# Kernel optimization log

Measured on AMD Instinct MI355X. Metric: run time of the kernel, lower is better.

The kernel has to match this reference:

```python
import jax, jax.numpy as jnp
import numpy as np

B, T, E, NH, VOCAB, MULT = 1, 1024, 768, 12, 32000, 32
N = E * MULT // NH  # 2048
LN_EPS = 1e-5


def setup_inputs() -> dict:
    key = jax.random.key(0)
    ks = jax.random.split(key, 6)
    return {
        "idx": jax.random.randint(ks[0], (B, T), 0, VOCAB),
        "embed": jax.random.normal(ks[1], (VOCAB, E), jnp.float32) * 0.02,
        "encoder": jax.random.normal(ks[2], (NH, E, N), jnp.float32) * 0.02,
        "encoder_v": jax.random.normal(ks[3], (NH, E, N), jnp.float32) * 0.02,
        "decoder": jax.random.normal(ks[4], (NH * N, E), jnp.float32) * 0.02,
        "lm_head": jax.random.normal(ks[5], (VOCAB, E), jnp.float32) * 0.02,
        "ln_w": jnp.ones((E,), jnp.float32),
        "ln_b": jnp.zeros((E,), jnp.float32),
        "n_layer": 6,
    }


def reference(idx, embed, encoder, encoder_v, decoder, lm_head, ln_w, ln_b, n_layer):
    nh, e, n = encoder.shape
    t = idx.shape[1]
    dec = decoder.reshape(nh, n, e)  # flatten order (h, n) -> h*N + n

    def ln(x):
        m = jnp.mean(x, axis=-1, keepdims=True)
        v = jnp.mean(jnp.square(x - m), axis=-1, keepdims=True)
        return (x - m) * jax.lax.rsqrt(v + LN_EPS) * ln_w + ln_b

    causal = jnp.tril(jnp.ones((t, t), bool))  # [T, T]
    scale = 1.0 / np.sqrt(n).astype(np.float32)

    x = ln(embed[idx])  # [B, T, E]  (the unsqueezed head dim broadcasts; keep it squeezed)
    for _ in range(n_layer):
        # encoder projection + ReLU: [B,T,E] x [H,E,N] -> [B,H,T,N]
        x_sparse = jax.nn.relu(jnp.einsum("bte,hen->bhtn", x, encoder))
        # hand-rolled causal attention, Q=K=x_sparse, V=x (broadcast over heads)
        scores = jnp.einsum("bhqn,bhkn->bhqk", x_sparse, x_sparse) * scale
        scores = jnp.where(causal, scores, -jnp.inf)
        attn = jax.nn.softmax(scores, axis=-1)
        y = jnp.einsum("bhqk,bke->bhqe", attn, x)  # [B,H,T,E]
        y = ln(y)
        y_sparse = jax.nn.relu(jnp.einsum("bhte,hen->bhtn", y, encoder_v))
        xy = x_sparse * y_sparse  # [B,H,T,N]; dropout p=0 -> identity
        y_mlp = jnp.einsum("bhtn,hne->bte", xy, dec)  # decoder matmul
        x = ln(x + ln(y_mlp))
    logits = jnp.einsum("bte,ve->btv", x, lm_head)
    return logits
```

## Files before the change

kernel.cpp:

```cpp
#include <hip/hip_runtime.h>

typedef unsigned short u16;
typedef short bf16x8 __attribute__((ext_vector_type(8)));
typedef float f32x4 __attribute__((ext_vector_type(4)));
typedef u16 u16x4 __attribute__((ext_vector_type(4)));

#define TT     1024
#define EE     768
#define NHH    12
#define ND     2048
#define VOC    32000
#define HNN    24576
#define NLAYER 6
#define LN_EPS 1e-5f
#define SPLITK 16

__device__ __forceinline__ float b2f(u16 u){
  unsigned int x = ((unsigned int)u) << 16; float f; __builtin_memcpy(&f, &x, 4); return f;
}
__device__ __forceinline__ u16 f2b(float f){
  unsigned int x; __builtin_memcpy(&x, &f, 4);
  x = x + 0x7fffu + ((x >> 16) & 1u);
  return (u16)(x >> 16);
}

__device__ __forceinline__ void gload16(const void* g, void* lds){
  __builtin_amdgcn_global_load_lds(
      (const __attribute__((address_space(1))) unsigned int*)g,
      (__attribute__((address_space(3))) unsigned int*)(unsigned int)(unsigned long long)lds,
      16, 0, 0);
}

__device__ __forceinline__ bf16x8 ldsr(unsigned addr){
  bf16x8 r;
  asm volatile("ds_read_b128 %0, %1" : "=v"(r) : "v"(addr));
  return r;
}

__device__ __forceinline__ void blk_sum2(float& a, float& b){
  #pragma unroll
  for (int o = 32; o > 0; o >>= 1){ a += __shfl_down(a, o); b += __shfl_down(b, o); }
  __shared__ float sa[4], sb[4];
  int lane = threadIdx.x & 63, wid = threadIdx.x >> 6;
  __syncthreads();
  if (lane == 0){ sa[wid] = a; sb[wid] = b; }
  __syncthreads();
  a = (sa[0] + sa[1]) + (sa[2] + sa[3]);
  b = (sb[0] + sb[1]) + (sb[2] + sb[3]);
}
__device__ __forceinline__ float blk_max(float v){
  #pragma unroll
  for (int o = 32; o > 0; o >>= 1) v = fmaxf(v, __shfl_down(v, o));
  __shared__ float sm[4];
  int lane = threadIdx.x & 63, wid = threadIdx.x >> 6;
  __syncthreads();
  if (lane == 0) sm[wid] = v;
  __syncthreads();
  return fmaxf(fmaxf(sm[0], sm[1]), fmaxf(sm[2], sm[3]));
}
__device__ __forceinline__ float blk_sum(float v){
  #pragma unroll
  for (int o = 32; o > 0; o >>= 1) v += __shfl_down(v, o);
  __shared__ float ss[4];
  int lane = threadIdx.x & 63, wid = threadIdx.x >> 6;
  __syncthreads();
  if (lane == 0) ss[wid] = v;
  __syncthreads();
  return (ss[0] + ss[1]) + (ss[2] + ss[3]);
}

__global__ void transpose_f2b(const float* __restrict__ in, long sIn,
                              u16* __restrict__ out, long sOut, int R, int Cc){
  __shared__ float tile[32][33];
  int z = blockIdx.z;
  in  += (long)z * sIn;
  out += (long)z * sOut;
  int c0 = blockIdx.x * 32, r0 = blockIdx.y * 32;
  int lx = threadIdx.x & 31, ly = threadIdx.x >> 5;
  #pragma unroll
  for (int i = 0; i < 32; i += 8)
    tile[ly + i][lx] = in[(long)(r0 + ly + i) * Cc + (c0 + lx)];
  __syncthreads();
  #pragma unroll
  for (int i = 0; i < 32; i += 8)
    out[(long)(c0 + ly + i) * R + (r0 + lx)] = f2b(tile[lx][ly + i]);
}

__global__ void conv_f2b(const float* __restrict__ in, u16* __restrict__ out){
  long i = ((long)blockIdx.x * 256 + threadIdx.x) * 4;
  float4 v = *(const float4*)(in + i);
  u16x4 o; o.x = f2b(v.x); o.y = f2b(v.y); o.z = f2b(v.z); o.w = f2b(v.w);
  *(u16x4*)(out + i) = o;
}

__global__ void embed_ln(const int* __restrict__ idx, const float* __restrict__ emb,
                         const float* __restrict__ w, const float* __restrict__ b,
                         float* __restrict__ xf, u16* __restrict__ xb, u16* __restrict__ xT){
  int t = blockIdx.x, tid = threadIdx.x;
  const float* src = emb + (long)idx[t] * EE;
  float v[3];
  #pragma unroll
  for (int j = 0; j < 3; j++) v[j] = src[tid + j * 256];
  float s = v[0] + v[1] + v[2];
  float s2 = v[0]*v[0] + v[1]*v[1] + v[2]*v[2];
  blk_sum2(s, s2);
  float m  = s * (1.0f / EE);
  float var = s2 * (1.0f / EE) - m * m;
  float rs = rsqrtf(var + LN_EPS);
  #pragma unroll
  for (int j = 0; j < 3; j++){
    int e = tid + j * 256;
    float o = (v[j] - m) * rs * w[e] + b[e];
    xf[(long)t * EE + e] = o;
    u16 ob = f2b(o);
    xb[(long)t * EE + e] = ob;
    xT[(long)e * TT + t] = ob;
  }
}

__global__ void ln_rows(const float* __restrict__ in, u16* __restrict__ out,
                        const float* __restrict__ w, const float* __restrict__ b){
  long row = blockIdx.x; int tid = threadIdx.x;
  const float* src = in + row * EE;
  float v[3];
  #pragma unroll
  for (int j = 0; j < 3; j++) v[j] = src[tid + j * 256];
  float s = v[0] + v[1] + v[2];
  float s2 = v[0]*v[0] + v[1]*v[1] + v[2]*v[2];
  blk_sum2(s, s2);
  float m = s * (1.0f / EE);
  float var = s2 * (1.0f / EE) - m * m;
  float rs = rsqrtf(var + LN_EPS);
  #pragma unroll
  for (int j = 0; j < 3; j++){
    int e = tid + j * 256;
    out[row * EE + e] = f2b((v[j] - m) * rs * w[e] + b[e]);
  }
}

__global__ void softmax_rows(const float* __restrict__ scores, u16* __restrict__ attn){
  int q = blockIdx.x, h = blockIdx.y, tid = threadIdx.x;
  const float* srow = scores + ((long)h * TT + q) * TT;
  u16* arow = attn + ((long)h * TT + q) * TT;
  float4 v = *(const float4*)(srow + tid * 4);
  float mx = blk_max(fmaxf(fmaxf(v.x, v.y), fmaxf(v.z, v.w)));
  float e0 = __expf(v.x - mx), e1 = __expf(v.y - mx);
  float e2 = __expf(v.z - mx), e3 = __expf(v.w - mx);
  float inv = 1.0f / blk_sum(e0 + e1 + e2 + e3);
  u16x4 o; o.x = f2b(e0 * inv); o.y = f2b(e1 * inv); o.z = f2b(e2 * inv); o.w = f2b(e3 * inv);
  *(u16x4*)(arow + tid * 4) = o;
}

template<int P>
__global__ void residual_ln(const float* __restrict__ part, const float* __restrict__ xin,
                            float* __restrict__ xf, u16* __restrict__ xb, u16* __restrict__ xT,
                            const float* __restrict__ w, const float* __restrict__ b){
  int t = blockIdx.x, tid = threadIdx.x;
  float g[3];
  #pragma unroll
  for (int j = 0; j < 3; j++){
    int e = tid + j * 256;
    float s = 0.f;
    #pragma unroll
    for (int pp = 0; pp < P; pp++) s += part[((long)pp * TT + t) * EE + e];
    g[j] = s;
  }
  float s = g[0] + g[1] + g[2], s2 = g[0]*g[0] + g[1]*g[1] + g[2]*g[2];
  blk_sum2(s, s2);
  float m = s * (1.0f / EE), var = s2 * (1.0f / EE) - m * m;
  float rs = rsqrtf(var + LN_EPS);
  float hh[3];
  #pragma unroll
  for (int j = 0; j < 3; j++){
    int e = tid + j * 256;
    hh[j] = xin[(long)t * EE + e] + ((g[j] - m) * rs * w[e] + b[e]);
  }
  s = hh[0] + hh[1] + hh[2]; s2 = hh[0]*hh[0] + hh[1]*hh[1] + hh[2]*hh[2];
  blk_sum2(s, s2);
  m = s * (1.0f / EE); var = s2 * (1.0f / EE) - m * m; rs = rsqrtf(var + LN_EPS);
  #pragma unroll
  for (int j = 0; j < 3; j++){
    int e = tid + j * 256;
    float o = (hh[j] - m) * rs * w[e] + b[e];
    xf[(long)t * EE + e] = o;
    u16 ob = f2b(o);
    xb[(long)t * EE + e] = ob;
    xT[(long)e * TT + t] = ob;
  }
}

template<int BM, int WM, int WN, int EPI, bool CCLAMP>
__global__ __launch_bounds__(WM*WN*64, (WM*WN*64 == 512) ? 2 : 3)
void gemm8p(const u16* __restrict__ Ab, long sA,
            const u16* __restrict__ Bb, long sB,
            void* __restrict__ Cb, long sC,
            int grid_m, int grid_mn,
            int K, int lda, int ldb, int ldc, float scale,
            const u16* __restrict__ Mul, long sMul, int ldmul){
  constexpr int BN = BM;
  constexpr int THREADS = WM*WN*64;
  constexpr int WMR = BM/WM, WNR = BN/WN;
  constexpr int MI = WMR/16, NI = WNR/16, MH = MI/2;
  constexpr unsigned BUFB   = (unsigned)(BM+BN)*64u;
  constexpr int      ROWS_RD = THREADS/4;
  constexpr unsigned ISSUE_B = (unsigned)THREADS*16u;
  __shared__ __align__(16) u16 S[3*BUFB/2];

  const int nwg = gridDim.x, orig = blockIdx.x;
  const int q = nwg >> 3, r = nwg & 7, xcd = orig & 7;
  const int wgid = (xcd < r ? xcd*(q+1) : r*(q+1) + (xcd - r)*q) + (orig >> 3);
  const int z   = wgid / grid_mn;
  const int rem = wgid - z*grid_mn;
  const int nb  = rem / grid_m;
  const int mb  = rem - nb*grid_m;
  const int m0 = mb*BM, n0 = nb*BN;
  const int tid = threadIdx.x, lane = tid & 63, wid = tid >> 6;

  if (EPI == 2 && n0 > m0 + (BM - 1)){
    float* C = (float*)Cb + (long)z * sC;
    constexpr int FIT = (BM*BN)/(THREADS*4);
    #pragma unroll
    for (int i = 0; i < FIT; i++){
      int idx4 = (tid + i*THREADS)*4;
      int rr = idx4 / BN, cc = idx4 - rr*BN;
      *(float4*)&C[(long)(m0+rr)*ldc + n0 + cc] = make_float4(-1e30f,-1e30f,-1e30f,-1e30f);
    }
    return;
  }

  const u16* A = Ab + (long)z*sA;
  const u16* B = Bb + (long)z*sB;

  const int rS = tid >> 2;
  const int cS = (((tid & 3) ^ (rS & 3)) << 3);
  const u16* gA[2]; const u16* gB[2];
  #pragma unroll
  for (int i = 0; i < 2; i++) gA[i] = A + (long)(m0 + i*ROWS_RD + rS)*lda + cS;
  #pragma unroll
  for (int i = 0; i < 2; i++) gB[i] = B + (long)(n0 + i*ROWS_RD + rS)*ldb + cS;

  char* Sb = (char*)&S[0];
  auto stageA = [&](int kt, unsigned bB){
    const int ko = kt << 5;
    gload16(gA[0] + ko, Sb + bB + wid*1024u);
    gload16(gA[1] + ko, Sb + bB + ISSUE_B + wid*1024u);
  };
  auto stageB = [&](int kt, unsigned bB){
    const int ko = kt << 5;
    gload16(gB[0] + ko, Sb + bB + (unsigned)BM*64u + wid*1024u);
    gload16(gB[1] + ko, Sb + bB + (unsigned)BM*64u + ISSUE_B + wid*1024u);
  };

  const int wr = wid / WN, wc = wid % WN;
  const int fr = lane & 15, fk = lane >> 4;
  const unsigned base = (unsigned)(unsigned long long)Sb;
  unsigned aAd[MI], bAd[NI];
  #pragma unroll
  for (int mi = 0; mi < MI; mi++){
    int row = wr*WMR + mi*16 + fr;
    aAd[mi] = base + (unsigned)(row*64 + ((fk ^ (row & 3)) << 4));
  }
  #pragma unroll
  for (int ni = 0; ni < NI; ni++){
    int row = wc*WNR + ni*16 + fr;
    bAd[ni] = base + (unsigned)BM*64u + (unsigned)(row*64 + ((fk ^ (row & 3)) << 4));
  }

  const int Keff = CCLAMP ? (m0 + BM < K ? m0 + BM : K) : K;
  const int NT = Keff >> 5;

  f32x4 acc[MI][NI] = {};

  stageA(0, 0); stageB(0, 0);
  stageA(1, BUFB); stageB(1, BUFB);
  asm volatile("s_waitcnt vmcnt(4)" ::: "memory");
  __builtin_amdgcn_s_barrier();
  __builtin_amdgcn_sched_barrier(0);

  unsigned rb = 0, wb = 2;
  for (int t = 0; t < NT; t++){
    const unsigned rbB = rb*BUFB, wbB = wb*BUFB;
    const int nx = (t + 2 < NT) ? t + 2 : NT - 1;
    bf16x8 bfr[NI], afr[MH];
    #pragma unroll
    for (int ni = 0; ni < NI; ni++) bfr[ni] = ldsr(bAd[ni] + rbB);
    #pragma unroll
    for (int u = 0; u < MH; u++)    afr[u]  = ldsr(aAd[u] + rbB);
    stageA(nx, wbB);
    __builtin_amdgcn_s_barrier();
    asm volatile("s_waitcnt lgkmcnt(0)" ::: "memory");
    __builtin_amdgcn_sched_barrier(0);
    __builtin_amdgcn_s_setprio(1);
    #pragma unroll
    for (int u = 0; u < MH; u++)
      #pragma unroll
      for (int ni = 0; ni < NI; ni++)
        acc[u][ni] = __builtin_amdgcn_mfma_f32_16x16x32_bf16(afr[u], bfr[ni], acc[u][ni], 0, 0, 0);
    __builtin_amdgcn_s_setprio(0);
    asm volatile("s_waitcnt vmcnt(4)" ::: "memory");
    __builtin_amdgcn_s_barrier();
    __builtin_amdgcn_sched_barrier(0);
    bf16x8 afr2[MH];
    #pragma unroll
    for (int u = 0; u < MH; u++) afr2[u] = ldsr(aAd[MH + u] + rbB);
    stageB(nx, wbB);
    __builtin_amdgcn_s_barrier();
    asm volatile("s_waitcnt lgkmcnt(0)" ::: "memory");
    __builtin_amdgcn_sched_barrier(0);
    __builtin_amdgcn_s_setprio(1);
    #pragma unroll
    for (int u = 0; u < MH; u++)
      #pragma unroll
      for (int ni = 0; ni < NI; ni++)
        acc[MH+u][ni] = __builtin_amdgcn_mfma_f32_16x16x32_bf16(afr2[u], bfr[ni], acc[MH+u][ni], 0, 0, 0);
    __builtin_amdgcn_s_setprio(0);
    asm volatile("s_waitcnt vmcnt(4)" ::: "memory");
    __builtin_amdgcn_s_barrier();
    __builtin_amdgcn_sched_barrier(0);
    rb = (rb + 1 == 3) ? 0 : rb + 1;
    wb = (wb + 1 == 3) ? 0 : wb + 1;
  }
  asm volatile("s_waitcnt vmcnt(0)" ::: "memory");

  const int er = (lane >> 4) * 4, ec = lane & 15;
  #pragma unroll
  for (int mi = 0; mi < MI; mi++){
    #pragma unroll
    for (int ni = 0; ni < NI; ni++){
      #pragma unroll
      for (int j = 0; j < 4; j++){
        int row = m0 + wr*WMR + mi*16 + er + j;
        int col = n0 + wc*WNR + ni*16 + ec;
        float v = acc[mi][ni][j];
        if (EPI == 0){
          ((float*)Cb + (long)z * sC)[(long)row * ldc + col] = v;
        } else if (EPI == 1){
          v = v > 0.f ? v : 0.f;
          ((u16*)Cb + (long)z * sC)[(long)row * ldc + col] = f2b(v);
        } else if (EPI == 2){
          v *= scale;
          if (col > row) v = -1e30f;
          ((float*)Cb + (long)z * sC)[(long)row * ldc + col] = v;
        } else {
          v = v > 0.f ? v : 0.f;
          float mfv = b2f((Mul + (long)z * sMul)[(long)row * ldmul + col]);
          ((u16*)Cb + (long)z * sC)[(long)row * ldc + col] = f2b(v * mfv);
        }
      }
    }
  }
}

extern "C" void kernel_launch(void* const* d_in, const int* in_sizes, int n_in,
                              void* d_out, int out_size, void* d_ws, size_t ws_size,
                              hipStream_t stream){
  (void)in_sizes; (void)n_in; (void)out_size; (void)ws_size;
  const int*   idx     = (const int*)  d_in[0];
  const float* embed   = (const float*)d_in[1];
  const float* encoder = (const float*)d_in[2];
  const float* encv    = (const float*)d_in[3];
  const float* decoder = (const float*)d_in[4];
  const float* lm_head = (const float*)d_in[5];
  const float* ln_w    = (const float*)d_in[6];
  const float* ln_b    = (const float*)d_in[7];
  float* out = (float*)d_out;

  char* p = (char*)d_ws;
  auto take = [&](size_t n){ char* r = p; p += (n + 255) & ~(size_t)255; return r; };
  u16*   encT  = (u16*)  take((size_t)NHH * ND * EE * 2);
  u16*   encvT = (u16*)  take((size_t)NHH * ND * EE * 2);
  u16*   decT  = (u16*)  take((size_t)EE * HNN * 2);
  u16*   lmhB  = (u16*)  take((size_t)VOC * EE * 2);
  float* xf    = (float*)take((size_t)TT * EE * 4);
  u16*   xb    = (u16*)  take((size_t)TT * EE * 2);
  u16*   xT    = (u16*)  take((size_t)EE * TT * 2);
  u16*   xs    = (u16*)  take((size_t)NHH * TT * ND * 2);
  char*  big   =         take((size_t)NHH * TT * TT * 4);
  u16*   attn  = (u16*)  take((size_t)NHH * TT * TT * 2);
  u16*   yb    = (u16*)  take((size_t)NHH * TT * EE * 2);
  take((size_t)8 * TT * EE * 4);
  float* scores = (float*)big;
  float* yf     = (float*)big;
  u16*   xy     = (u16*)big;
  float* part   = (float*)attn;

  dim3 blk(256, 1, 1);

  transpose_f2b<<<dim3(ND / 32, EE / 32, NHH), blk, 0, stream>>>(encoder, (long)EE * ND, encT,  (long)ND * EE, EE, ND);
  transpose_f2b<<<dim3(ND / 32, EE / 32, NHH), blk, 0, stream>>>(encv,    (long)EE * ND, encvT, (long)ND * EE, EE, ND);
  transpose_f2b<<<dim3(EE / 32, HNN / 32, 1),  blk, 0, stream>>>(decoder, 0, decT, 0, HNN, EE);
  conv_f2b<<<dim3((VOC * EE) / 1024, 1, 1), blk, 0, stream>>>(lm_head, lmhB);

  embed_ln<<<dim3(TT, 1, 1), blk, 0, stream>>>(idx, embed, ln_w, ln_b, xf, xb, xT);

  const float scl = 0.022097086912079608f;

  for (int L = 0; L < NLAYER; ++L){
    gemm8p<256,2,4,1,false><<<dim3(4*8*NHH), dim3(512), 0, stream>>>(
        xb, 0, encT, (long)ND * EE, xs, (long)TT * ND,
        4, 32, EE, EE, EE, ND, 0.f, (const u16*)0, 0, 0);
    gemm8p<256,2,4,2,false><<<dim3(4*4*NHH), dim3(512), 0, stream>>>(
        xs, (long)TT * ND, xs, (long)TT * ND, scores, (long)TT * TT,
        4, 16, ND, ND, ND, TT, scl, (const u16*)0, 0, 0);
    softmax_rows<<<dim3(TT, NHH, 1), blk, 0, stream>>>(scores, attn);
    gemm8p<128,2,2,0,true><<<dim3(8*6*NHH), blk, 0, stream>>>(
        attn, (long)TT * TT, xT, 0, yf, (long)TT * EE,
        8, 48, TT, TT, TT, EE, 0.f, (const u16*)0, 0, 0);
    ln_rows<<<dim3(NHH * TT, 1, 1), blk, 0, stream>>>(yf, yb, ln_w, ln_b);
    gemm8p<256,2,4,3,false><<<dim3(4*8*NHH), dim3(512), 0, stream>>>(
        yb, (long)TT * EE, encvT, (long)ND * EE, xy, (long)ND,
        4, 32, EE, EE, EE, HNN, 0.f, xs, (long)TT * ND, ND);
    gemm8p<128,2,2,0,false><<<dim3(8*6*SPLITK), blk, 0, stream>>>(
        xy, (long)(HNN / SPLITK), decT, (long)(HNN / SPLITK), part, (long)TT * EE,
        8, 48, HNN / SPLITK, HNN, HNN, EE, 0.f, (const u16*)0, 0, 0);
    residual_ln<SPLITK><<<dim3(TT, 1, 1), blk, 0, stream>>>(part, xf, xf, xb, xT, ln_w, ln_b);
  }

  gemm8p<256,2,4,0,false><<<dim3(4*125), dim3(512), 0, stream>>>(
      xb, 0, lmhB, 0, out, 0,
      4, 500, EE, EE, EE, VOC, 0.f, (const u16*)0, 0, 0);
}
```

Measured before the change: 1.996 ms.

## Replace 256-tile GEMMs with single-phase 128-tile kernel and staggered K start

Replaces the templated GEMM, which used 256x256 tiles with 512 threads for the big GEMMs and two MFMA phases per k-step, with a fixed 128x128, 256-thread kernel that does one phase per k-step: it stages A and B together, then loads all fragments and issues 16 MFMAs. Each block also starts its K loop at a different offset (a hash of its tile indices), so concurrent blocks spread their reads across different K slices. The smaller tiles quadruple the grid for the encoder, score and lm_head GEMMs, trading per-tile data reuse for more parallelism and occupancy. Rotating the K order changes the float summation order slightly.

Result: slower. 2.139 ms (+7.1%).

```diff
diff --git a/kernel.cpp b/kernel.cpp
--- a/kernel.cpp
+++ b/kernel.cpp
@@ -189,22 +189,16 @@
   }
 }
 
-template<int BM, int WM, int WN, int EPI, bool CCLAMP>
-__global__ __launch_bounds__(WM*WN*64, (WM*WN*64 == 512) ? 2 : 3)
-void gemm8p(const u16* __restrict__ Ab, long sA,
+template<int EPI, bool CCLAMP>
+__global__ __launch_bounds__(256, 3)
+void gemm1p(const u16* __restrict__ Ab, long sA,
             const u16* __restrict__ Bb, long sB,
             void* __restrict__ Cb, long sC,
             int grid_m, int grid_mn,
             int K, int lda, int ldb, int ldc, float scale,
             const u16* __restrict__ Mul, long sMul, int ldmul){
-  constexpr int BN = BM;
-  constexpr int THREADS = WM*WN*64;
-  constexpr int WMR = BM/WM, WNR = BN/WN;
-  constexpr int MI = WMR/16, NI = WNR/16, MH = MI/2;
-  constexpr unsigned BUFB   = (unsigned)(BM+BN)*64u;
-  constexpr int      ROWS_RD = THREADS/4;
-  constexpr unsigned ISSUE_B = (unsigned)THREADS*16u;
-  __shared__ __align__(16) u16 S[3*BUFB/2];
+  constexpr unsigned BUFB = 16384u;
+  __shared__ __align__(16) u16 S[3 * 8192];
 
   const int nwg = gridDim.x, orig = blockIdx.x;
   const int q = nwg >> 3, r = nwg & 7, xcd = orig & 7;
@@ -213,16 +207,15 @@
   const int rem = wgid - z*grid_mn;
   const int nb  = rem / grid_m;
   const int mb  = rem - nb*grid_m;
-  const int m0 = mb*BM, n0 = nb*BN;
+  const int m0 = mb*128, n0 = nb*128;
   const int tid = threadIdx.x, lane = tid & 63, wid = tid >> 6;
 
-  if (EPI == 2 && n0 > m0 + (BM - 1)){
+  if (EPI == 2 && n0 > m0 + 127){
     float* C = (float*)Cb + (long)z * sC;
-    constexpr int FIT = (BM*BN)/(THREADS*4);
-    #pragma unroll
-    for (int i = 0; i < FIT; i++){
-      int idx4 = (tid + i*THREADS)*4;
-      int rr = idx4 / BN, cc = idx4 - rr*BN;
+    #pragma unroll
+    for (int i = 0; i < 16; i++){
+      int idx4 = (tid + i*256)*4;
+      int rr = idx4 >> 7, cc = idx4 & 127;
       *(float4*)&C[(long)(m0+rr)*ldc + n0 + cc] = make_float4(-1e30f,-1e30f,-1e30f,-1e30f);
     }
     return;
@@ -235,102 +228,85 @@
   const int cS = (((tid & 3) ^ (rS & 3)) << 3);
   const u16* gA[2]; const u16* gB[2];
   #pragma unroll
-  for (int i = 0; i < 2; i++) gA[i] = A + (long)(m0 + i*ROWS_RD + rS)*lda + cS;
-  #pragma unroll
-  for (int i = 0; i < 2; i++) gB[i] = B + (long)(n0 + i*ROWS_RD + rS)*ldb + cS;
+  for (int i = 0; i < 2; i++) gA[i] = A + (long)(m0 + i*64 + rS)*lda + cS;
+  #pragma unroll
+  for (int i = 0; i < 2; i++) gB[i] = B + (long)(n0 + i*64 + rS)*ldb + cS;
 
   char* Sb = (char*)&S[0];
-  auto stageA = [&](int kt, unsigned bB){
+  auto stage = [&](int kt, unsigned bB){
     const int ko = kt << 5;
-    gload16(gA[0] + ko, Sb + bB + wid*1024u);
-    gload16(gA[1] + ko, Sb + bB + ISSUE_B + wid*1024u);
+    gload16(gA[0] + ko, Sb + bB +          wid*1024u);
+    gload16(gA[1] + ko, Sb + bB +  4096u + wid*1024u);
+    gload16(gB[0] + ko, Sb + bB +  8192u + wid*1024u);
+    gload16(gB[1] + ko, Sb + bB + 12288u + wid*1024u);
   };
-  auto stageB = [&](int kt, unsigned bB){
-    const int ko = kt << 5;
-    gload16(gB[0] + ko, Sb + bB + (unsigned)BM*64u + wid*1024u);
-    gload16(gB[1] + ko, Sb + bB + (unsigned)BM*64u + ISSUE_B + wid*1024u);
-  };
-
-  const int wr = wid / WN, wc = wid % WN;
+
+  const int wr = wid >> 1, wc = wid & 1;
   const int fr = lane & 15, fk = lane >> 4;
   const unsigned base = (unsigned)(unsigned long long)Sb;
-  unsigned aAd[MI], bAd[NI];
-  #pragma unroll
-  for (int mi = 0; mi < MI; mi++){
-    int row = wr*WMR + mi*16 + fr;
+  unsigned aAd[4], bAd[4];
+  #pragma unroll
+  for (int mi = 0; mi < 4; mi++){
+    int row = wr*64 + mi*16 + fr;
     aAd[mi] = base + (unsigned)(row*64 + ((fk ^ (row & 3)) << 4));
   }
   #pragma unroll
-  for (int ni = 0; ni < NI; ni++){
-    int row = wc*WNR + ni*16 + fr;
-    bAd[ni] = base + (unsigned)BM*64u + (unsigned)(row*64 + ((fk ^ (row & 3)) << 4));
-  }
-
-  const int Keff = CCLAMP ? (m0 + BM < K ? m0 + BM : K) : K;
+  for (int ni = 0; ni < 4; ni++){
+    int row = wc*64 + ni*16 + fr;
+    bAd[ni] = base + 8192u + (unsigned)(row*64 + ((fk ^ (row & 3)) << 4));
+  }
+
+  const int Keff = CCLAMP ? (m0 + 128 < K ? m0 + 128 : K) : K;
   const int NT = Keff >> 5;
-
-  f32x4 acc[MI][NI] = {};
-
-  stageA(0, 0); stageB(0, 0);
-  stageA(1, BUFB); stageB(1, BUFB);
+  const int s0 = (mb*13 + nb*7 + z*5) % NT;
+
+  f32x4 acc[4][4] = {};
+
+  int p1 = s0 + 1; if (p1 >= NT) p1 -= NT;
+  stage(s0, 0);
+  stage(p1, BUFB);
   asm volatile("s_waitcnt vmcnt(4)" ::: "memory");
   __builtin_amdgcn_s_barrier();
   __builtin_amdgcn_sched_barrier(0);
 
-  unsigned rb = 0, wb = 2;
+  unsigned rbB = 0, wbB = 2u*BUFB;
   for (int t = 0; t < NT; t++){
-    const unsigned rbB = rb*BUFB, wbB = wb*BUFB;
-    const int nx = (t + 2 < NT) ? t + 2 : NT - 1;
-    bf16x8 bfr[NI], afr[MH];
-    #pragma unroll
-    for (int ni = 0; ni < NI; ni++) bfr[ni] = ldsr(bAd[ni] + rbB);
-    #pragma unroll
-    for (int u = 0; u < MH; u++)    afr[u]  = ldsr(aAd[u] + rbB);
-    stageA(nx, wbB);
+    int nx = (t + 2 < NT) ? t + 2 : NT - 1;
+    int ph = s0 + nx; if (ph >= NT) ph -= NT;
+    stage(ph, wbB);
+    bf16x8 afr[4], bfr[4];
+    #pragma unroll
+    for (int ni = 0; ni < 4; ni++) bfr[ni] = ldsr(bAd[ni] + rbB);
+    #pragma unroll
+    for (int mi = 0; mi < 4; mi++) afr[mi] = ldsr(aAd[mi] + rbB);
     __builtin_amdgcn_s_barrier();
     asm volatile("s_waitcnt lgkmcnt(0)" ::: "memory");
     __builtin_amdgcn_sched_barrier(0);
     __builtin_amdgcn_s_setprio(1);
     #pragma unroll
-    for (int u = 0; u < MH; u++)
+    for (int mi = 0; mi < 4; mi++)
       #pragma unroll
-      for (int ni = 0; ni < NI; ni++)
-        acc[u][ni] = __builtin_amdgcn_mfma_f32_16x16x32_bf16(afr[u], bfr[ni], acc[u][ni], 0, 0, 0);
+      for (int ni = 0; ni < 4; ni++)
+        acc[mi][ni] = __builtin_amdgcn_mfma_f32_16x16x32_bf16(afr[mi], bfr[ni], acc[mi][ni], 0, 0, 0);
     __builtin_amdgcn_s_setprio(0);
+    __builtin_amdgcn_sched_barrier(0);
     asm volatile("s_waitcnt vmcnt(4)" ::: "memory");
     __builtin_amdgcn_s_barrier();
     __builtin_amdgcn_sched_barrier(0);
-    bf16x8 afr2[MH];
-    #pragma unroll
-    for (int u = 0; u < MH; u++) afr2[u] = ldsr(aAd[MH + u] + rbB);
-    stageB(nx, wbB);
-    __builtin_amdgcn_s_barrier();
-    asm volatile("s_waitcnt lgkmcnt(0)" ::: "memory");
-    __builtin_amdgcn_sched_barrier(0);
-    __builtin_amdgcn_s_setprio(1);
-    #pragma unroll
-    for (int u = 0; u < MH; u++)
-      #pragma unroll
-      for (int ni = 0; ni < NI; ni++)
-        acc[MH+u][ni] = __builtin_amdgcn_mfma_f32_16x16x32_bf16(afr2[u], bfr[ni], acc[MH+u][ni], 0, 0, 0);
-    __builtin_amdgcn_s_setprio(0);
-    asm volatile("s_waitcnt vmcnt(4)" ::: "memory");
-    __builtin_amdgcn_s_barrier();
-    __builtin_amdgcn_sched_barrier(0);
-    rb = (rb + 1 == 3) ? 0 : rb + 1;
-    wb = (wb + 1 == 3) ? 0 : wb + 1;
+    unsigned tmp = rbB; rbB += BUFB; if (rbB == 3u*BUFB) rbB = 0;
+    wbB = tmp;
   }
   asm volatile("s_waitcnt vmcnt(0)" ::: "memory");
 
   const int er = (lane >> 4) * 4, ec = lane & 15;
   #pragma unroll
-  for (int mi = 0; mi < MI; mi++){
-    #pragma unroll
-    for (int ni = 0; ni < NI; ni++){
+  for (int mi = 0; mi < 4; mi++){
+    #pragma unroll
+    for (int ni = 0; ni < 4; ni++){
       #pragma unroll
       for (int j = 0; j < 4; j++){
-        int row = m0 + wr*WMR + mi*16 + er + j;
-        int col = n0 + wc*WNR + ni*16 + ec;
+        int row = m0 + wr*64 + mi*16 + er + j;
+        int col = n0 + wc*64 + ni*16 + ec;
         float v = acc[mi][ni][j];
         if (EPI == 0){
           ((float*)Cb + (long)z * sC)[(long)row * ldc + col] = v;
@@ -396,27 +372,27 @@
   const float scl = 0.022097086912079608f;
 
   for (int L = 0; L < NLAYER; ++L){
-    gemm8p<256,2,4,1,false><<<dim3(4*8*NHH), dim3(512), 0, stream>>>(
+    gemm1p<1,false><<<dim3(8*16*NHH), blk, 0, stream>>>(
         xb, 0, encT, (long)ND * EE, xs, (long)TT * ND,
-        4, 32, EE, EE, EE, ND, 0.f, (const u16*)0, 0, 0);
-    gemm8p<256,2,4,2,false><<<dim3(4*4*NHH), dim3(512), 0, stream>>>(
+        8, 128, EE, EE, EE, ND, 0.f, (const u16*)0, 0, 0);
+    gemm1p<2,false><<<dim3(8*8*NHH), blk, 0, stream>>>(
         xs, (long)TT * ND, xs, (long)TT * ND, scores, (long)TT * TT,
-        4, 16, ND, ND, ND, TT, scl, (const u16*)0, 0, 0);
+        8, 64, ND, ND, ND, TT, scl, (const u16*)0, 0, 0);
     softmax_rows<<<dim3(TT, NHH, 1), blk, 0, stream>>>(scores, attn);
-    gemm8p<128,2,2,0,true><<<dim3(8*6*NHH), blk, 0, stream>>>(
+    gemm1p<0,true><<<dim3(8*6*NHH), blk, 0, stream>>>(
         attn, (long)TT * TT, xT, 0, yf, (long)TT * EE,
         8, 48, TT, TT, TT, EE, 0.f, (const u16*)0, 0, 0);
     ln_rows<<<dim3(NHH * TT, 1, 1), blk, 0, stream>>>(yf, yb, ln_w, ln_b);
-    gemm8p<256,2,4,3,false><<<dim3(4*8*NHH), dim3(512), 0, stream>>>(
+    gemm1p<3,false><<<dim3(8*16*NHH), blk, 0, stream>>>(
         yb, (long)TT * EE, encvT, (long)ND * EE, xy, (long)ND,
-        4, 32, EE, EE, EE, HNN, 0.f, xs, (long)TT * ND, ND);
-    gemm8p<128,2,2,0,false><<<dim3(8*6*SPLITK), blk, 0, stream>>>(
+        8, 128, EE, EE, EE, HNN, 0.f, xs, (long)TT * ND, ND);
+    gemm1p<0,false><<<dim3(8*6*SPLITK), blk, 0, stream>>>(
         xy, (long)(HNN / SPLITK), decT, (long)(HNN / SPLITK), part, (long)TT * EE,
         8, 48, HNN / SPLITK, HNN, HNN, EE, 0.f, (const u16*)0, 0, 0);
     residual_ln<SPLITK><<<dim3(TT, 1, 1), blk, 0, stream>>>(part, xf, xf, xb, xT, ln_w, ln_b);
   }
 
-  gemm8p<256,2,4,0,false><<<dim3(4*125), dim3(512), 0, stream>>>(
+  gemm1p<0,false><<<dim3(8*250), blk, 0, stream>>>(
       xb, 0, lmhB, 0, out, 0,
-      4, 500, EE, EE, EE, VOC, 0.f, (const u16*)0, 0, 0);
-}
+      8, 2000, EE, EE, EE, VOC, 0.f, (const u16*)0, 0, 0);
+}
```
